# Kernel tuning notes

Hardware: AMD Instinct MI355X
Metric: run time of the kernel (lower is better)

The kernel has to match this reference:

```python
import jax, jax.numpy as jnp
import numpy as np


def gcn_layer(x, W, b, src, dst):
    """PyG GCNConv with improved=True: A_hat = A + 2I, D^-1/2 A_hat D^-1/2 X W + b."""
    n = x.shape[0]
    xw = x @ W  # [N, H]
    # degree counts each incoming edge (weight 1) plus self-loop weight 2
    deg = jnp.zeros((n,), x.dtype).at[dst].add(jnp.ones((src.shape[0],), x.dtype)) + 2.0
    dinv = jax.lax.rsqrt(deg)  # deg >= 2 always
    norm = (dinv[src] * dinv[dst])[:, None]  # [E, 1]
    agg = jax.ops.segment_sum(xw[src] * norm, dst, num_segments=n)  # scatter-add to dst
    agg = agg + (2.0 * dinv * dinv)[:, None] * xw  # self-loop contribution (weight 2)
    return agg + b


def xavier(k, shape):
    lim = (6.0 / (shape[0] + shape[1])) ** 0.5
    return jax.random.uniform(k, shape, jnp.float32, -lim, lim)


def setup_inputs() -> dict:
    key = jax.random.key(0)
    ks = jax.random.split(key, 8)
    N, E, D = 100_000, 1_600_000, 64  # nodes, edges, features_dim
    H1, H2 = 64, 64                   # gnn_dims
    M1, M2 = 128, 64                  # ind_pol_dims
    rep = jax.random.normal(ks[0], (N, D), jnp.float32)
    edge_index = jax.random.randint(ks[1], (2, E), 0, N, jnp.int32)
    return {
        "rep": rep,
        "edge_index": edge_index,
        "W1": xavier(ks[2], (D, H1)), "b1": jnp.zeros((H1,), jnp.float32),
        "W2": xavier(ks[3], (H1, H2)), "b2": jnp.zeros((H2,), jnp.float32),
        "Wa": xavier(ks[4], (H2 + D, M1)), "ba": jnp.zeros((M1,), jnp.float32),
        "Wb": xavier(ks[5], (M1, M2)), "bb": jnp.zeros((M2,), jnp.float32),
        "Wo": xavier(ks[6], (M2, 1)), "bo": jnp.zeros((1,), jnp.float32),
    }


def reference(rep, edge_index, W1, b1, W2, b2, Wa, ba, Wb, bb, Wo, bo):
    src, dst = edge_index[0], edge_index[1]
    # eval mode: f.dropout(training=False) is identity
    h = jax.nn.relu(gcn_layer(rep, W1, b1, src, dst))
    h = jax.nn.relu(gcn_layer(h, W2, b2, src, dst))
    z = jnp.concatenate([rep, h], axis=1)  # [N, D + H2]
    z = jax.nn.relu(z @ Wa + ba)
    z = jax.nn.relu(z @ Wb + bb)
    prob = jax.nn.sigmoid(z @ Wo + bo)[:, 0]  # [N]
    # gumbel_softmax(hard=True, tau=1) over logits = [1-p, p] (torch semantics:
    # probabilities fed directly as logits, as in the original code)
    logits = jnp.stack([1.0 - prob, prob], axis=1)  # [N, 2]
    u = jax.random.uniform(jax.random.key(42), logits.shape, jnp.float32, 1e-20, 1.0)
    g = -jnp.log(-jnp.log(u))
    y = jax.nn.softmax(logits + g, axis=1)
    hard = jax.nn.one_hot(jnp.argmax(y, axis=1), 2, dtype=y.dtype)
    st = hard + y - jax.lax.stop_gradient(y)  # straight-through
    ind = st @ jnp.array([[0.0], [1.0]], dtype=y.dtype)  # mm with [[0],[1]]
    return (prob, ind[:, 0])
```

## Files before the change

### kernel.cpp

```cpp
#include <hip/hip_runtime.h>
#include <math.h>


__device__ __forceinline__ unsigned rotl32(unsigned x, int r) {
  return (x << r) | (x >> (32 - r));
}

__device__ __forceinline__ void threefry2x32(unsigned k0, unsigned k1,
                                             unsigned x0, unsigned x1,
                                             unsigned& o0, unsigned& o1) {
  unsigned ks2 = k0 ^ k1 ^ 0x1BD11BDAu;
#define TF_RND(r) { x0 += x1; x1 = rotl32(x1, (r)); x1 ^= x0; }
  x0 += k0; x1 += k1;
  TF_RND(13) TF_RND(15) TF_RND(26) TF_RND(6)
  x0 += k1; x1 += ks2 + 1u;
  TF_RND(17) TF_RND(29) TF_RND(16) TF_RND(24)
  x0 += ks2; x1 += k0 + 2u;
  TF_RND(13) TF_RND(15) TF_RND(26) TF_RND(6)
  x0 += k0; x1 += k1 + 3u;
  TF_RND(17) TF_RND(29) TF_RND(16) TF_RND(24)
  x0 += k1; x1 += ks2 + 4u;
  TF_RND(13) TF_RND(15) TF_RND(26) TF_RND(6)
  x0 += ks2; x1 += k0 + 5u;
#undef TF_RND
  o0 = x0; o1 = x1;
}

__device__ __forceinline__ unsigned jax_random_bits_u32(unsigned k0, unsigned k1,
                                                        unsigned flat_idx) {
  unsigned a, b;
  threefry2x32(k0, k1, 0u, flat_idx, a, b);
  return a ^ b;
}

#define BSHIFT 8
#define BMASK 255

__global__ __launch_bounds__(256) void coarse_hist_kernel(
    const int* __restrict__ dst, int* __restrict__ coarse, int E) {
  __shared__ int h[512];
  for (int i = threadIdx.x; i < 512; i += 256) h[i] = 0;
  __syncthreads();
  for (int e = blockIdx.x * blockDim.x + threadIdx.x; e < E;
       e += gridDim.x * blockDim.x)
    atomicAdd(&h[dst[e] >> BSHIFT], 1);
  __syncthreads();
  for (int i = threadIdx.x; i < 512; i += 256)
    if (h[i]) atomicAdd(&coarse[i], h[i]);
}

__global__ __launch_bounds__(512) void coarse_scan_kernel(
    const int* __restrict__ coarse, int* __restrict__ bbase,
    int* __restrict__ cbase, int NBUCK) {
  __shared__ int sh[512];
  int t = threadIdx.x;
  int v = (t < NBUCK) ? coarse[t] : 0;
  sh[t] = v;
  __syncthreads();
  for (int o = 1; o < 512; o <<= 1) {
    int a = (t >= o) ? sh[t - o] : 0;
    __syncthreads();
    sh[t] += a;
    __syncthreads();
  }
  if (t < NBUCK) {
    int ex = sh[t] - v;
    bbase[t] = ex;
    cbase[t] = ex;
    if (t == NBUCK - 1) bbase[NBUCK] = sh[t];
  }
}

#define CHUNK 4096
__global__ __launch_bounds__(256) void bucket_scatter_kernel(
    const int* __restrict__ src, const int* __restrict__ dst,
    int* __restrict__ cbase, int* __restrict__ pkB, int E) {
  __shared__ int sS[CHUNK];
  __shared__ int dS[CHUNK];
  __shared__ int cnt[512];
  __shared__ int base[512];
  const int t = threadIdx.x;
  const int e0 = blockIdx.x * CHUNK;
  const int n = min(CHUNK, E - e0);
  for (int i = t; i < 512; i += 256) cnt[i] = 0;
  for (int i = t; i < n; i += 256) {
    sS[i] = src[e0 + i];
    dS[i] = dst[e0 + i];
  }
  __syncthreads();
  for (int i = t; i < n; i += 256) atomicAdd(&cnt[dS[i] >> BSHIFT], 1);
  __syncthreads();
  for (int i = t; i < 512; i += 256) {
    int c = cnt[i];
    base[i] = c ? atomicAdd(&cbase[i], c) : 0;
  }
  __syncthreads();
  for (int i = t; i < 512; i += 256) cnt[i] = 0;
  __syncthreads();
  for (int i = t; i < n; i += 256) {
    int d = dS[i];
    int b = d >> BSHIFT;
    int r = atomicAdd(&cnt[b], 1);
    pkB[base[b] + r] = ((d & BMASK) << 20) | sS[i];
  }
}

__global__ __launch_bounds__(256) void bucket_finalize_kernel(
    const int* __restrict__ pkB, const int* __restrict__ bbase,
    int* __restrict__ off, float* __restrict__ dinv, int* __restrict__ srcS,
    int N) {
  __shared__ int cnt[256];
  __shared__ int sh[256];
  const int t = threadIdx.x;
  const int b = blockIdx.x;
  const int lo = bbase[b], hi = bbase[b + 1];
  cnt[t] = 0;
  __syncthreads();
  for (int i = lo + t; i < hi; i += 256) atomicAdd(&cnt[pkB[i] >> 20], 1);
  __syncthreads();
  const int deg = cnt[t];
  sh[t] = deg;
  __syncthreads();
  for (int o = 1; o < 256; o <<= 1) {
    int a = (t >= o) ? sh[t - o] : 0;
    __syncthreads();
    sh[t] += a;
    __syncthreads();
  }
  const int ex = sh[t] - deg;
  const int node = (b << BSHIFT) + t;
  if (node < N) {
    off[node] = lo + ex;
    dinv[node] = 1.0f / sqrtf((float)deg + 2.0f);
    if (node == N - 1) off[N] = hi;
  }
  cnt[t] = lo + ex;
  __syncthreads();
  for (int i = lo + t; i < hi; i += 256) {
    int u = pkB[i];
    int pos = atomicAdd(&cnt[u >> 20], 1);
    srcS[pos] = u & 0xFFFFF;
  }
}

__global__ __launch_bounds__(256) void aggregate_kernel(
    const float* __restrict__ xws, const int* __restrict__ srcS,
    const int* __restrict__ off, const float* __restrict__ dinv,
    const float* __restrict__ bias, float* __restrict__ h, int N) {
  int node = (blockIdx.x * blockDim.x + threadIdx.x) >> 6;
  int f = threadIdx.x & 63;
  if (node >= N) return;
  int beg = off[node], end = off[node + 1];
  float a0 = 0.f, a1 = 0.f, a2 = 0.f, a3 = 0.f;
  int e = beg;
  for (; e + 4 <= end; e += 4) {
    int s0 = srcS[e], s1 = srcS[e + 1], s2 = srcS[e + 2], s3 = srcS[e + 3];
    a0 += xws[(size_t)s0 * 64 + f];
    a1 += xws[(size_t)s1 * 64 + f];
    a2 += xws[(size_t)s2 * 64 + f];
    a3 += xws[(size_t)s3 * 64 + f];
  }
  for (; e < end; ++e) a0 += xws[(size_t)srcS[e] * 64 + f];
  float acc = (a0 + a1) + (a2 + a3);
  float di = dinv[node];
  float v = di * (acc + 2.0f * xws[(size_t)node * 64 + f]) + bias[f];
  h[(size_t)node * 64 + f] = fmaxf(v, 0.0f);
}

__global__ __launch_bounds__(256) void gemm64v2_kernel(
    const float* __restrict__ X, const float* __restrict__ W,
    const float* __restrict__ dinv, float* __restrict__ Y, int N, int flags) {
  __shared__ float Ws[64 * 64];
  __shared__ float Xs[64 * 68];
  const int t = threadIdx.x;
  {
    const float4* W4 = (const float4*)W;
    float4* Ws4 = (float4*)Ws;
    for (int i = t; i < 16 * 64; i += 256) Ws4[i] = W4[i];
  }
  const int row0 = blockIdx.x * 64;
  for (int i = t; i < 64 * 16; i += 256) {
    int r = i >> 4, c4 = i & 15;
    int gr = row0 + r;
    float4 v = make_float4(0.f, 0.f, 0.f, 0.f);
    if (gr < N) v = *(const float4*)&X[(size_t)gr * 64 + c4 * 4];
    *(float4*)&Xs[r * 68 + c4 * 4] = v;
  }
  __syncthreads();

  const int tx = t & 15, ty = t >> 4;
  const int c0 = tx * 4;
  const int r0 = ty * 4;
  float acc[4][4];
#pragma unroll
  for (int i = 0; i < 4; ++i)
#pragma unroll
    for (int j = 0; j < 4; ++j) acc[i][j] = 0.f;

#pragma unroll 4
  for (int k4 = 0; k4 < 16; ++k4) {
    float4 xv[4];
#pragma unroll
    for (int i = 0; i < 4; ++i)
      xv[i] = *(const float4*)&Xs[(r0 + i) * 68 + k4 * 4];
#pragma unroll
    for (int kk = 0; kk < 4; ++kk) {
      float w[4];
#pragma unroll
      for (int j = 0; j < 4; ++j) w[j] = Ws[(k4 * 4 + kk) * 64 + c0 + j];
      const float xk[4] = {
          kk == 0 ? xv[0].x : kk == 1 ? xv[0].y : kk == 2 ? xv[0].z : xv[0].w,
          kk == 0 ? xv[1].x : kk == 1 ? xv[1].y : kk == 2 ? xv[1].z : xv[1].w,
          kk == 0 ? xv[2].x : kk == 1 ? xv[2].y : kk == 2 ? xv[2].z : xv[2].w,
          kk == 0 ? xv[3].x : kk == 1 ? xv[3].y : kk == 2 ? xv[3].z : xv[3].w};
#pragma unroll
      for (int i = 0; i < 4; ++i)
#pragma unroll
        for (int j = 0; j < 4; ++j) acc[i][j] = fmaf(xk[i], w[j], acc[i][j]);
    }
  }

#pragma unroll
  for (int i = 0; i < 4; ++i) {
    int gr = row0 + r0 + i;
    if (gr >= N) continue;
    float sc = (flags & 8) ? dinv[gr] : 1.0f;
    float4 v = make_float4(acc[i][0], acc[i][1], acc[i][2], acc[i][3]);
    if (flags & 8) { v.x *= sc; v.y *= sc; v.z *= sc; v.w *= sc; }
    *(float4*)&Y[(size_t)gr * 64 + c0] = v;
  }
}

#define XP 132
__global__ __launch_bounds__(256, 4) void head_mega_kernel(
    const float* __restrict__ rep, const float* __restrict__ h2,
    const float* __restrict__ Wa, const float* __restrict__ ba,
    const float* __restrict__ Wb, const float* __restrict__ bb,
    const float* __restrict__ Wo, const float* __restrict__ bo,
    float* __restrict__ out, int N) {
  __shared__ float smem[64 * XP + 16 * 68];
  float* Xs = smem;
  float* red = smem + 64 * XP;
  const int t = threadIdx.x;
  const int row0 = blockIdx.x * 64;

  for (int i = t; i < 2048; i += 256) {
    int r = i >> 5, c4 = i & 31;
    int gr = row0 + r;
    float4 v = make_float4(0.f, 0.f, 0.f, 0.f);
    if (gr < N)
      v = (c4 < 16) ? *(const float4*)&rep[(size_t)gr * 64 + c4 * 4]
                    : *(const float4*)&h2[(size_t)gr * 64 + (c4 - 16) * 4];
    *(float4*)&Xs[r * XP + c4 * 4] = v;
  }
  __syncthreads();

  const int tx = t & 15, ty = t >> 4;
  const int c0 = tx * 8;
  const int r0 = ty * 4;
  float za[4][8];
#pragma unroll
  for (int i = 0; i < 4; ++i)
#pragma unroll
    for (int j = 0; j < 8; ++j) za[i][j] = 0.f;

#pragma unroll 2
  for (int k = 0; k < 128; ++k) {
    float x[4];
#pragma unroll
    for (int i = 0; i < 4; ++i) x[i] = Xs[(r0 + i) * XP + k];
    float4 w0 = *(const float4*)&Wa[k * 128 + c0];
    float4 w1 = *(const float4*)&Wa[k * 128 + c0 + 4];
    const float w[8] = {w0.x, w0.y, w0.z, w0.w, w1.x, w1.y, w1.z, w1.w};
#pragma unroll
    for (int i = 0; i < 4; ++i)
#pragma unroll
      for (int j = 0; j < 8; ++j) za[i][j] = fmaf(x[i], w[j], za[i][j]);
  }
#pragma unroll
  for (int i = 0; i < 4; ++i)
#pragma unroll
    for (int j = 0; j < 8; ++j)
      za[i][j] = fmaxf(za[i][j] + ba[c0 + j], 0.f);

  __syncthreads();
  float* zaS = Xs;
#pragma unroll
  for (int i = 0; i < 4; ++i) {
    *(float4*)&zaS[(r0 + i) * XP + c0] =
        make_float4(za[i][0], za[i][1], za[i][2], za[i][3]);
    *(float4*)&zaS[(r0 + i) * XP + c0 + 4] =
        make_float4(za[i][4], za[i][5], za[i][6], za[i][7]);
  }
  __syncthreads();

  const int c0b = tx * 4;
  float zb[4][4];
#pragma unroll
  for (int i = 0; i < 4; ++i)
#pragma unroll
    for (int j = 0; j < 4; ++j) zb[i][j] = 0.f;
#pragma unroll 4
  for (int k = 0; k < 128; ++k) {
    float x[4];
#pragma unroll
    for (int i = 0; i < 4; ++i) x[i] = zaS[(r0 + i) * XP + k];
    float4 w = *(const float4*)&Wb[k * 64 + c0b];
    const float wj[4] = {w.x, w.y, w.z, w.w};
#pragma unroll
    for (int i = 0; i < 4; ++i)
#pragma unroll
      for (int j = 0; j < 4; ++j) zb[i][j] = fmaf(x[i], wj[j], zb[i][j]);
  }
  float part[4];
#pragma unroll
  for (int i = 0; i < 4; ++i) {
    part[i] = 0.f;
#pragma unroll
    for (int j = 0; j < 4; ++j) {
      float v = fmaxf(zb[i][j] + bb[c0b + j], 0.f);
      part[i] = fmaf(v, Wo[c0b + j], part[i]);
    }
  }
  __syncthreads();
#pragma unroll
  for (int i = 0; i < 4; ++i) red[tx * 68 + r0 + i] = part[i];
  __syncthreads();
  if (t < 64) {
    int gr = row0 + t;
    if (gr < N) {
      float s = 0.f;
#pragma unroll
      for (int u = 0; u < 16; ++u) s += red[u * 68 + t];
      float w = s + bo[0];
      float p = 1.0f / (1.0f + expf(-w));
      unsigned i = (unsigned)gr;
      unsigned bits0 = jax_random_bits_u32(0u, 42u, 2u * i);
      unsigned bits1 = jax_random_bits_u32(0u, 42u, 2u * i + 1u);
      float f0 = __uint_as_float((bits0 >> 9) | 0x3f800000u) - 1.0f;
      float f1 = __uint_as_float((bits1 >> 9) | 0x3f800000u) - 1.0f;
      float u0 = fmaxf(1e-20f, f0 + 1e-20f);
      float u1 = fmaxf(1e-20f, f1 + 1e-20f);
      float g0 = -logf(-logf(u0));
      float g1 = -logf(-logf(u1));
      float a0 = (1.0f - p) + g0;
      float a1 = p + g1;
      float m = fmaxf(a0, a1);
      float e0 = expf(a0 - m), e1 = expf(a1 - m);
      float ssum = e0 + e1;
      float y0 = e0 / ssum, y1 = e1 / ssum;
      float hard1 = (y1 > y0) ? 1.0f : 0.0f;
      float st1 = (hard1 + y1) - y1;
      out[gr] = p;
      out[N + gr] = st1;
    }
  }
}

extern "C" void kernel_launch(void* const* d_in, const int* in_sizes, int n_in,
                              void* d_out, int out_size, void* d_ws, size_t ws_size,
                              hipStream_t stream) {
  const float* rep = (const float*)d_in[0];
  const int* ei = (const int*)d_in[1];
  const float* W1 = (const float*)d_in[2];
  const float* b1 = (const float*)d_in[3];
  const float* W2 = (const float*)d_in[4];
  const float* b2 = (const float*)d_in[5];
  const float* Wa = (const float*)d_in[6];
  const float* ba = (const float*)d_in[7];
  const float* Wb = (const float*)d_in[8];
  const float* bb = (const float*)d_in[9];
  const float* Wo = (const float*)d_in[10];
  const float* bo = (const float*)d_in[11];
  float* out = (float*)d_out;

  const int N = in_sizes[0] / 64;
  const int E = in_sizes[1] / 2;
  const int* srcI = ei;
  const int* dstI = ei + E;

  const int NBUCK = (N + 255) >> BSHIFT;

  float* ws = (float*)d_ws;
  float* bufA = ws;
  float* bufB = bufA + (size_t)N * 64;
  float* dinv = bufB + (size_t)N * 64;
  int* coarse = (int*)(dinv + N);
  int* bbase = coarse + 512;
  int* cbase = bbase + 513;
  int* off = cbase + 512;
  int* pkB = off + N + 1;
  int* srcS = pkB + E;

  const int nb64 = (N + 63) / 64;
  const int nbW = (N + 3) / 4;
  const int nbA = (E + CHUNK - 1) / CHUNK;

  hipMemsetAsync(coarse, 0, 512 * 4, stream);
  coarse_hist_kernel<<<256, 256, 0, stream>>>(dstI, coarse, E);
  coarse_scan_kernel<<<1, 512, 0, stream>>>(coarse, bbase, cbase, NBUCK);
  bucket_scatter_kernel<<<nbA, 256, 0, stream>>>(srcI, dstI, cbase, pkB, E);
  bucket_finalize_kernel<<<NBUCK, 256, 0, stream>>>(pkB, bbase, off, dinv,
                                                    srcS, N);

  gemm64v2_kernel<<<nb64, 256, 0, stream>>>(rep, W1, dinv, bufA, N, 8);
  aggregate_kernel<<<nbW, 256, 0, stream>>>(bufA, srcS, off, dinv, b1, bufB, N);

  gemm64v2_kernel<<<nb64, 256, 0, stream>>>(bufB, W2, dinv, bufA, N, 8);
  aggregate_kernel<<<nbW, 256, 0, stream>>>(bufA, srcS, off, dinv, b2, bufB, N);

  head_mega_kernel<<<nb64, 256, 0, stream>>>(rep, bufB, Wa, ba, Wb, bb, Wo, bo,
                                             out, N);
}
```

Before: 410.4 us.

## Vectorize GCN aggregation with float2 half-waves; stage head weights in LDS

The aggregate kernel now splits each 64-lane wave into two halves. Each half gathers a different edge's source row as float2, and the halves are combined with a cross-half shuffle, so fewer edge iterations are needed per node. The head MLP kernel now copies Wa (in two 64-row chunks) and Wb into shared memory instead of reading them from global memory in the inner loops. It replaces the padded shared layout with an XOR-style rotated swizzle to avoid bank conflicts and drops the occupancy hint from launch bounds. The larger shared-memory footprint may lower occupancy, and the added chunk synchronizations cost some time.

Result: slower. 441.7 us (+7.6%).

```diff
diff --git a/kernel.cpp b/kernel.cpp
--- a/kernel.cpp
+++ b/kernel.cpp
@@ -148,23 +148,40 @@
     const int* __restrict__ off, const float* __restrict__ dinv,
     const float* __restrict__ bias, float* __restrict__ h, int N) {
   int node = (blockIdx.x * blockDim.x + threadIdx.x) >> 6;
-  int f = threadIdx.x & 63;
+  int lane = threadIdx.x & 63;
+  int half = lane >> 5;
+  int fp = lane & 31;
   if (node >= N) return;
+  const float2* xw2 = (const float2*)xws;
   int beg = off[node], end = off[node + 1];
-  float a0 = 0.f, a1 = 0.f, a2 = 0.f, a3 = 0.f;
+  float2 s0 = make_float2(0.f, 0.f), s1 = make_float2(0.f, 0.f);
   int e = beg;
   for (; e + 4 <= end; e += 4) {
-    int s0 = srcS[e], s1 = srcS[e + 1], s2 = srcS[e + 2], s3 = srcS[e + 3];
-    a0 += xws[(size_t)s0 * 64 + f];
-    a1 += xws[(size_t)s1 * 64 + f];
-    a2 += xws[(size_t)s2 * 64 + f];
-    a3 += xws[(size_t)s3 * 64 + f];
-  }
-  for (; e < end; ++e) a0 += xws[(size_t)srcS[e] * 64 + f];
-  float acc = (a0 + a1) + (a2 + a3);
-  float di = dinv[node];
-  float v = di * (acc + 2.0f * xws[(size_t)node * 64 + f]) + bias[f];
-  h[(size_t)node * 64 + f] = fmaxf(v, 0.0f);
+    int sA = srcS[e + half];
+    int sB = srcS[e + 2 + half];
+    float2 vA = xw2[(size_t)sA * 32 + fp];
+    float2 vB = xw2[(size_t)sB * 32 + fp];
+    s0.x += vA.x; s0.y += vA.y;
+    s1.x += vB.x; s1.y += vB.y;
+  }
+  for (; e < end; e += 2) {
+    if (e + half < end) {
+      float2 v = xw2[(size_t)srcS[e + half] * 32 + fp];
+      s0.x += v.x; s0.y += v.y;
+    }
+  }
+  float tx = s0.x + s1.x, ty = s0.y + s1.y;
+  tx += __shfl_xor(tx, 32, 64);
+  ty += __shfl_xor(ty, 32, 64);
+  if (half == 0) {
+    float di = dinv[node];
+    float2 self = xw2[(size_t)node * 32 + fp];
+    float2 b = ((const float2*)bias)[fp];
+    float2 r;
+    r.x = fmaxf(di * (tx + 2.0f * self.x) + b.x, 0.f);
+    r.y = fmaxf(di * (ty + 2.0f * self.y) + b.y, 0.f);
+    *(float2*)&h[(size_t)node * 64 + fp * 2] = r;
+  }
 }
 
 __global__ __launch_bounds__(256) void gemm64v2_kernel(
@@ -231,16 +248,15 @@
   }
 }
 
-#define XP 132
-__global__ __launch_bounds__(256, 4) void head_mega_kernel(
+__global__ __launch_bounds__(256) void head_mega_kernel(
     const float* __restrict__ rep, const float* __restrict__ h2,
     const float* __restrict__ Wa, const float* __restrict__ ba,
     const float* __restrict__ Wb, const float* __restrict__ bb,
     const float* __restrict__ Wo, const float* __restrict__ bo,
     float* __restrict__ out, int N) {
-  __shared__ float smem[64 * XP + 16 * 68];
+  __shared__ float smem[16384];
   float* Xs = smem;
-  float* red = smem + 64 * XP;
+  float* Wbuf = smem + 8192;
   const int t = threadIdx.x;
   const int row0 = blockIdx.x * 64;
 
@@ -251,9 +267,9 @@
     if (gr < N)
       v = (c4 < 16) ? *(const float4*)&rep[(size_t)gr * 64 + c4 * 4]
                     : *(const float4*)&h2[(size_t)gr * 64 + (c4 - 16) * 4];
-    *(float4*)&Xs[r * XP + c4 * 4] = v;
-  }
-  __syncthreads();
+    int scol = (c4 * 4 + ((r >> 2) << 2)) & 127;
+    *(float4*)&Xs[r * 128 + scol] = v;
+  }
 
   const int tx = t & 15, ty = t >> 4;
   const int c0 = tx * 8;
@@ -264,18 +280,28 @@
 #pragma unroll
     for (int j = 0; j < 8; ++j) za[i][j] = 0.f;
 
+  for (int chunk = 0; chunk < 2; ++chunk) {
+    __syncthreads();
+    const float4* Wa4 = (const float4*)(Wa + chunk * 64 * 128);
+    float4* Wd = (float4*)Wbuf;
+    for (int i = t; i < 2048; i += 256) Wd[i] = Wa4[i];
+    __syncthreads();
+    const int kb = chunk * 64;
 #pragma unroll 2
-  for (int k = 0; k < 128; ++k) {
-    float x[4];
-#pragma unroll
-    for (int i = 0; i < 4; ++i) x[i] = Xs[(r0 + i) * XP + k];
-    float4 w0 = *(const float4*)&Wa[k * 128 + c0];
-    float4 w1 = *(const float4*)&Wa[k * 128 + c0 + 4];
-    const float w[8] = {w0.x, w0.y, w0.z, w0.w, w1.x, w1.y, w1.z, w1.w};
-#pragma unroll
-    for (int i = 0; i < 4; ++i)
-#pragma unroll
-      for (int j = 0; j < 8; ++j) za[i][j] = fmaf(x[i], w[j], za[i][j]);
+    for (int kk = 0; kk < 64; ++kk) {
+      const int k = kb + kk;
+      const int kc = (k + (ty << 2)) & 127;
+      float x[4];
+#pragma unroll
+      for (int i = 0; i < 4; ++i) x[i] = Xs[(r0 + i) * 128 + kc];
+      float4 w0 = *(const float4*)&Wbuf[kk * 128 + c0];
+      float4 w1 = *(const float4*)&Wbuf[kk * 128 + c0 + 4];
+      const float w[8] = {w0.x, w0.y, w0.z, w0.w, w1.x, w1.y, w1.z, w1.w};
+#pragma unroll
+      for (int i = 0; i < 4; ++i)
+#pragma unroll
+        for (int j = 0; j < 8; ++j) za[i][j] = fmaf(x[i], w[j], za[i][j]);
+    }
   }
 #pragma unroll
   for (int i = 0; i < 4; ++i)
@@ -285,12 +311,22 @@
 
   __syncthreads();
   float* zaS = Xs;
-#pragma unroll
-  for (int i = 0; i < 4; ++i) {
-    *(float4*)&zaS[(r0 + i) * XP + c0] =
-        make_float4(za[i][0], za[i][1], za[i][2], za[i][3]);
-    *(float4*)&zaS[(r0 + i) * XP + c0 + 4] =
-        make_float4(za[i][4], za[i][5], za[i][6], za[i][7]);
+  {
+    int s0 = (c0 + (ty << 2)) & 127;
+    int s1 = (c0 + 4 + (ty << 2)) & 127;
+#pragma unroll
+    for (int i = 0; i < 4; ++i) {
+      *(float4*)&zaS[(r0 + i) * 128 + s0] =
+          make_float4(za[i][0], za[i][1], za[i][2], za[i][3]);
+      *(float4*)&zaS[(r0 + i) * 128 + s1] =
+          make_float4(za[i][4], za[i][5], za[i][6], za[i][7]);
+    }
+  }
+  __syncthreads();
+  {
+    const float4* Wbg = (const float4*)Wb;
+    float4* Wd = (float4*)Wbuf;
+    for (int i = t; i < 2048; i += 256) Wd[i] = Wbg[i];
   }
   __syncthreads();
 
@@ -302,10 +338,11 @@
     for (int j = 0; j < 4; ++j) zb[i][j] = 0.f;
 #pragma unroll 4
   for (int k = 0; k < 128; ++k) {
+    const int kc = (k + (ty << 2)) & 127;
     float x[4];
 #pragma unroll
-    for (int i = 0; i < 4; ++i) x[i] = zaS[(r0 + i) * XP + k];
-    float4 w = *(const float4*)&Wb[k * 64 + c0b];
+    for (int i = 0; i < 4; ++i) x[i] = zaS[(r0 + i) * 128 + kc];
+    float4 w = *(const float4*)&Wbuf[k * 64 + c0b];
     const float wj[4] = {w.x, w.y, w.z, w.w};
 #pragma unroll
     for (int i = 0; i < 4; ++i)
@@ -323,6 +360,7 @@
     }
   }
   __syncthreads();
+  float* red = Wbuf;
 #pragma unroll
   for (int i = 0; i < 4; ++i) red[tx * 68 + r0 + i] = part[i];
   __syncthreads();
```

## Stage head MLP weights in LDS with swizzled activations; unroll aggregation by 8

Applied to the files above, without the earlier changes.

The head kernel now copies chunks of Wa and Wb into a shared-memory buffer instead of reading weights from global memory inside the k-loop. The activation tile uses a rotated (swizzled) column layout in place of row padding to avoid bank conflicts, and each thread's output columns are split into low and high halves. The GCN aggregation loop is unrolled to eight independent gathers to raise memory-level parallelism. This adds extra barriers per chunk and drops the occupancy hint of 4 in launch_bounds, which may change register allocation.

Result: no change. 417.5 us (+1.7%).

```diff
diff --git a/kernel.cpp b/kernel.cpp
--- a/kernel.cpp
+++ b/kernel.cpp
@@ -152,16 +152,22 @@
   if (node >= N) return;
   int beg = off[node], end = off[node + 1];
   float a0 = 0.f, a1 = 0.f, a2 = 0.f, a3 = 0.f;
+  float a4 = 0.f, a5 = 0.f, a6 = 0.f, a7 = 0.f;
   int e = beg;
-  for (; e + 4 <= end; e += 4) {
-    int s0 = srcS[e], s1 = srcS[e + 1], s2 = srcS[e + 2], s3 = srcS[e + 3];
+  for (; e + 8 <= end; e += 8) {
+    int s0 = srcS[e],     s1 = srcS[e + 1], s2 = srcS[e + 2], s3 = srcS[e + 3];
+    int s4 = srcS[e + 4], s5 = srcS[e + 5], s6 = srcS[e + 6], s7 = srcS[e + 7];
     a0 += xws[(size_t)s0 * 64 + f];
     a1 += xws[(size_t)s1 * 64 + f];
     a2 += xws[(size_t)s2 * 64 + f];
     a3 += xws[(size_t)s3 * 64 + f];
+    a4 += xws[(size_t)s4 * 64 + f];
+    a5 += xws[(size_t)s5 * 64 + f];
+    a6 += xws[(size_t)s6 * 64 + f];
+    a7 += xws[(size_t)s7 * 64 + f];
   }
   for (; e < end; ++e) a0 += xws[(size_t)srcS[e] * 64 + f];
-  float acc = (a0 + a1) + (a2 + a3);
+  float acc = ((a0 + a1) + (a2 + a3)) + ((a4 + a5) + (a6 + a7));
   float di = dinv[node];
   float v = di * (acc + 2.0f * xws[(size_t)node * 64 + f]) + bias[f];
   h[(size_t)node * 64 + f] = fmaxf(v, 0.0f);
@@ -231,16 +237,14 @@
   }
 }
 
-#define XP 132
-__global__ __launch_bounds__(256, 4) void head_mega_kernel(
+__global__ __launch_bounds__(256) void head_mega_kernel(
     const float* __restrict__ rep, const float* __restrict__ h2,
     const float* __restrict__ Wa, const float* __restrict__ ba,
     const float* __restrict__ Wb, const float* __restrict__ bb,
     const float* __restrict__ Wo, const float* __restrict__ bo,
     float* __restrict__ out, int N) {
-  __shared__ float smem[64 * XP + 16 * 68];
-  float* Xs = smem;
-  float* red = smem + 64 * XP;
+  __shared__ float Xs[64 * 128];
+  __shared__ float Wbuf[32 * 128];
   const int t = threadIdx.x;
   const int row0 = blockIdx.x * 64;
 
@@ -251,12 +255,13 @@
     if (gr < N)
       v = (c4 < 16) ? *(const float4*)&rep[(size_t)gr * 64 + c4 * 4]
                     : *(const float4*)&h2[(size_t)gr * 64 + (c4 - 16) * 4];
-    *(float4*)&Xs[r * XP + c4 * 4] = v;
-  }
-  __syncthreads();
+    int scol = (c4 * 4 + ((r >> 2) << 2)) & 127;
+    *(float4*)&Xs[r * 128 + scol] = v;
+  }
 
   const int tx = t & 15, ty = t >> 4;
-  const int c0 = tx * 8;
+  const int cL = tx * 4;
+  const int cH = 64 + tx * 4;
   const int r0 = ty * 4;
   float za[4][8];
 #pragma unroll
@@ -264,35 +269,50 @@
 #pragma unroll
     for (int j = 0; j < 8; ++j) za[i][j] = 0.f;
 
+  for (int chunk = 0; chunk < 4; ++chunk) {
+    __syncthreads();
+    const float4* Wa4 = (const float4*)(Wa + chunk * 32 * 128);
+    float4* Wd = (float4*)Wbuf;
+    for (int i = t; i < 1024; i += 256) Wd[i] = Wa4[i];
+    __syncthreads();
+    const int kb = chunk * 32;
 #pragma unroll 2
-  for (int k = 0; k < 128; ++k) {
-    float x[4];
-#pragma unroll
-    for (int i = 0; i < 4; ++i) x[i] = Xs[(r0 + i) * XP + k];
-    float4 w0 = *(const float4*)&Wa[k * 128 + c0];
-    float4 w1 = *(const float4*)&Wa[k * 128 + c0 + 4];
-    const float w[8] = {w0.x, w0.y, w0.z, w0.w, w1.x, w1.y, w1.z, w1.w};
-#pragma unroll
-    for (int i = 0; i < 4; ++i)
-#pragma unroll
-      for (int j = 0; j < 8; ++j) za[i][j] = fmaf(x[i], w[j], za[i][j]);
-  }
-#pragma unroll
-  for (int i = 0; i < 4; ++i)
-#pragma unroll
-    for (int j = 0; j < 8; ++j)
-      za[i][j] = fmaxf(za[i][j] + ba[c0 + j], 0.f);
+    for (int kk = 0; kk < 32; ++kk) {
+      const int kc = (kb + kk + (ty << 2)) & 127;
+      float x[4];
+#pragma unroll
+      for (int i = 0; i < 4; ++i) x[i] = Xs[(r0 + i) * 128 + kc];
+      float4 w0 = *(const float4*)&Wbuf[kk * 128 + cL];
+      float4 w1 = *(const float4*)&Wbuf[kk * 128 + cH];
+      const float w[8] = {w0.x, w0.y, w0.z, w0.w, w1.x, w1.y, w1.z, w1.w};
+#pragma unroll
+      for (int i = 0; i < 4; ++i)
+#pragma unroll
+        for (int j = 0; j < 8; ++j) za[i][j] = fmaf(x[i], w[j], za[i][j]);
+    }
+  }
+#pragma unroll
+  for (int i = 0; i < 4; ++i) {
+#pragma unroll
+    for (int j = 0; j < 4; ++j) {
+      za[i][j] = fmaxf(za[i][j] + ba[cL + j], 0.f);
+      za[i][4 + j] = fmaxf(za[i][4 + j] + ba[cH + j], 0.f);
+    }
+  }
 
   __syncthreads();
   float* zaS = Xs;
-#pragma unroll
-  for (int i = 0; i < 4; ++i) {
-    *(float4*)&zaS[(r0 + i) * XP + c0] =
-        make_float4(za[i][0], za[i][1], za[i][2], za[i][3]);
-    *(float4*)&zaS[(r0 + i) * XP + c0 + 4] =
-        make_float4(za[i][4], za[i][5], za[i][6], za[i][7]);
-  }
-  __syncthreads();
+  {
+    int sL = (cL + (ty << 2)) & 127;
+    int sH = (cH + (ty << 2)) & 127;
+#pragma unroll
+    for (int i = 0; i < 4; ++i) {
+      *(float4*)&zaS[(r0 + i) * 128 + sL] =
+          make_float4(za[i][0], za[i][1], za[i][2], za[i][3]);
+      *(float4*)&zaS[(r0 + i) * 128 + sH] =
+          make_float4(za[i][4], za[i][5], za[i][6], za[i][7]);
+    }
+  }
 
   const int c0b = tx * 4;
   float zb[4][4];
@@ -300,17 +320,27 @@
   for (int i = 0; i < 4; ++i)
 #pragma unroll
     for (int j = 0; j < 4; ++j) zb[i][j] = 0.f;
+
+  for (int chunk = 0; chunk < 2; ++chunk) {
+    __syncthreads();
+    const float4* Wb4 = (const float4*)(Wb + chunk * 64 * 64);
+    float4* Wd = (float4*)Wbuf;
+    for (int i = t; i < 1024; i += 256) Wd[i] = Wb4[i];
+    __syncthreads();
+    const int kb = chunk * 64;
 #pragma unroll 4
-  for (int k = 0; k < 128; ++k) {
-    float x[4];
-#pragma unroll
-    for (int i = 0; i < 4; ++i) x[i] = zaS[(r0 + i) * XP + k];
-    float4 w = *(const float4*)&Wb[k * 64 + c0b];
-    const float wj[4] = {w.x, w.y, w.z, w.w};
-#pragma unroll
-    for (int i = 0; i < 4; ++i)
-#pragma unroll
-      for (int j = 0; j < 4; ++j) zb[i][j] = fmaf(x[i], wj[j], zb[i][j]);
+    for (int kk = 0; kk < 64; ++kk) {
+      const int kc = (kb + kk + (ty << 2)) & 127;
+      float x[4];
+#pragma unroll
+      for (int i = 0; i < 4; ++i) x[i] = zaS[(r0 + i) * 128 + kc];
+      float4 w = *(const float4*)&Wbuf[kk * 64 + c0b];
+      const float wj[4] = {w.x, w.y, w.z, w.w};
+#pragma unroll
+      for (int i = 0; i < 4; ++i)
+#pragma unroll
+        for (int j = 0; j < 4; ++j) zb[i][j] = fmaf(x[i], wj[j], zb[i][j]);
+    }
   }
   float part[4];
 #pragma unroll
@@ -323,6 +353,7 @@
     }
   }
   __syncthreads();
+  float* red = Wbuf;
 #pragma unroll
   for (int i = 0; i < 4; ++i) red[tx * 68 + r0 + i] = part[i];
   __syncthreads();
```
